# Optimization experiments

Hardware: AMD Instinct MI355X
Metric: run time of the kernel (lower is better)

Reference implementation:

```python
import jax, jax.numpy as jnp
import numpy as np

M_POS = 0.5
M_NEG_SIM = 0.1
LAM_NEG = 1.0


def setup_inputs() -> dict:
    key = jax.random.key(0)
    N, d, G = 8192, 1024, 64
    codebook = jax.random.normal(key, (N, d), dtype=jnp.float32)
    base = (jnp.arange(N) // G) * G  # contiguous groups of size G (vq_to_range)
    starts = base.astype(jnp.int32)
    ends = (base + G - 1).astype(jnp.int32)
    return {"codebook": codebook, "starts": starts, "ends": ends, "max_i": N - 1}


def reference(codebook, starts, ends, max_i):
    N, d = codebook.shape
    M = min(N, int(max_i) + 1)  # rows processed by the python loop

    # cosine similarity rows [0:M] vs all N
    zn = codebook / jnp.linalg.norm(codebook, axis=-1, keepdims=True)
    cos = jnp.einsum('md,nd->mn', zn[:M], zn)  # (M, N)

    # pairwise Euclidean distances rows [0:M] vs all N via ||a-b||^2 = |a|^2+|b|^2-2ab
    sq = jnp.sum(codebook * codebook, axis=-1)  # (N,)
    dot = jnp.einsum('md,nd->mn', codebook[:M], codebook)  # (M, N)
    d2 = jnp.maximum(sq[:M, None] + sq[None, :] - 2.0 * dot, 0.0)

    j = jnp.arange(N)[None, :]
    i = jnp.arange(M)[:, None]
    in_range = (j >= starts[:M, None]) & (j <= ends[:M, None])
    pos_mask = in_range & (j != i)
    # original: group_mask[i]=False then neg = ~group_mask, so i is in negatives
    neg_mask = (~in_range) | (j == i)

    pos_cnt = jnp.sum(pos_mask, axis=-1)
    neg_cnt = jnp.sum(neg_mask, axis=-1)

    # safe sqrt: only evaluate on positive-mask entries
    D = jnp.sqrt(jnp.where(pos_mask, d2, 1.0))
    pos_term = jnp.square(jax.nn.relu(D - M_POS)) * pos_mask
    pos_pull = jnp.sum(pos_term, axis=-1) / jnp.maximum(pos_cnt, 1)

    neg_cos = jnp.clip(cos, -1.0, 1.0)
    neg_term = jnp.square(jax.nn.relu(jnp.abs(neg_cos) - M_NEG_SIM)) * neg_mask
    ortho = jnp.sum(neg_term, axis=-1) / jnp.maximum(neg_cnt, 1)

    valid = (pos_cnt > 0) & (neg_cnt > 0)
    per_row = jnp.where(valid, pos_pull + LAM_NEG * ortho, 0.0)
    cnt = jnp.sum(valid)
    total = jnp.sum(per_row)
    return jnp.where(cnt > 0, total / jnp.maximum(cnt, 1).astype(total.dtype), jnp.zeros((), total.dtype))
```

## Files before the change

### kernel.cpp

```cpp
#include <hip/hip_runtime.h>
#include <hip/hip_bf16.h>
#include <stdint.h>

#define M_POS 0.5f
#define M_NEG 0.1f
#define LAM_NEG 1.0f

typedef __attribute__((ext_vector_type(4))) float floatx4;
typedef __attribute__((ext_vector_type(8))) int   intx8;

union Frag8 { intx8 v; int4 q[2]; };

__global__ __launch_bounds__(256) void prep_kernel(
    const float* __restrict__ cb, unsigned char* __restrict__ cb_q,
    float* __restrict__ sq, float* __restrict__ inv_norm,
    unsigned* __restrict__ zero_base, int zero_len,
    int N, int d)
{
    const int gi = blockIdx.x * 256 + threadIdx.x;
    if (gi < zero_len) zero_base[gi] = 0u;

    const int row = blockIdx.x;
    const float* src = cb + (size_t)row * d;
    unsigned char* dst = cb_q + (size_t)row * d;
    const int t = threadIdx.x;

    float s = 0.f;
    for (int c = t * 4; c < d; c += 1024) {
        float4 v = *(const float4*)(src + c);
        s += v.x * v.x + v.y * v.y + v.z * v.z + v.w * v.w;
        int pk = __builtin_amdgcn_cvt_pk_fp8_f32(v.x, v.y, 0, false);
        pk     = __builtin_amdgcn_cvt_pk_fp8_f32(v.z, v.w, pk, true);
        *(int*)(dst + c) = pk;
    }
    for (int o = 32; o > 0; o >>= 1) s += __shfl_down(s, o, 64);
    __shared__ float wsum[4];
    if ((t & 63) == 0) wsum[t >> 6] = s;
    __syncthreads();
    if (t == 0) {
        float tot = wsum[0] + wsum[1] + wsum[2] + wsum[3];
        sq[row] = tot;
        inv_norm[row] = rsqrtf(tot);
    }
}

__global__ __launch_bounds__(256, 2) void gram_loss_kernel(
    const unsigned char* __restrict__ A,
    const float* __restrict__ sq, const float* __restrict__ inv_norm,
    const int* __restrict__ starts, const int* __restrict__ ends,
    const int* __restrict__ max_ip,
    float* __restrict__ pos_acc, float* __restrict__ neg_acc,
    unsigned* __restrict__ counter, float* __restrict__ out,
    int N, int d)
{
    const int M = min(N, max_ip[0] + 1);

    int vt = blockIdx.x;
    const int nB = gridDim.x;
    if ((nB & 7) == 0) {
        const int per = nB >> 3;
        vt = (blockIdx.x & 7) * per + (blockIdx.x >> 3);
    }

    int bx = (int)((sqrtf(8.f * (float)vt + 1.f) - 1.f) * 0.5f);
    while ((bx + 1) * (bx + 2) / 2 <= vt) bx++;
    while (bx * (bx + 1) / 2 > vt) bx--;
    const int by = vt - bx * (bx + 1) / 2;

    const int rowBase = by * 128;
    const int colBase = bx * 128;
    const bool isDiag = (by == bx);

    __shared__ alignas(16) unsigned char ldsA[2][128 * 128];
    __shared__ alignas(16) unsigned char ldsB[2][128 * 128];

    const int tid  = threadIdx.x;
    const int wave = tid >> 6;
    const int lane = tid & 63;
    const int wr = (wave >> 1) * 64;
    const int wc = (wave & 1) * 64;

    floatx4 acc[4][4];
#pragma unroll
    for (int a = 0; a < 4; ++a)
#pragma unroll
        for (int b = 0; b < 4; ++b) acc[a][b] = (floatx4){0.f, 0.f, 0.f, 0.f};

    const int sRow = lane >> 3;
    const int sChk = lane & 7;
    const int srcOffC = ((sChk ^ sRow) * 16);
    const int kTiles = d / 128;

    const int rl = lane & 15;
    const int g  = lane >> 4;
    const int rx = rl & 7;
    const int c0 = (((2 * g)     ^ rx) * 16);
    const int c1 = (((2 * g + 1) ^ rx) * 16);

#define STAGE(BUF, KT)                                                          \
    { const int k0_ = (KT) * 128;                                               \
      _Pragma("unroll")                                                         \
      for (int h = 0; h < 4; ++h) {                                             \
        const int r_ = wave * 32 + h * 8 + sRow;                                \
        const unsigned char* ga_ = A + (size_t)(rowBase + r_) * d + k0_ + srcOffC; \
        const unsigned char* gb_ = A + (size_t)(colBase + r_) * d + k0_ + srcOffC; \
        __builtin_amdgcn_global_load_lds(                                       \
            (const __attribute__((address_space(1))) void*)ga_,                 \
            (__attribute__((address_space(3))) void*)(ldsA[BUF] + r_ * 128 + sChk * 16), 16, 0, 0); \
        __builtin_amdgcn_global_load_lds(                                       \
            (const __attribute__((address_space(1))) void*)gb_,                 \
            (__attribute__((address_space(3))) void*)(ldsB[BUF] + r_ * 128 + sChk * 16), 16, 0, 0); \
      } }

    STAGE(0, 0)
    asm volatile("s_waitcnt vmcnt(0)" ::: "memory");
    __builtin_amdgcn_s_barrier();

    int cur = 0;
    for (int kt = 0; kt < kTiles; ++kt) {
        const bool more = (kt + 1 < kTiles);
        if (more) {
            if (cur == 0) STAGE(1, kt + 1)
            else          STAGE(0, kt + 1)
        }

        Frag8 af[4], bf[4];
#pragma unroll
        for (int t4 = 0; t4 < 4; ++t4) {
            const unsigned char* pa = ldsA[cur] + (wr + t4 * 16 + rl) * 128;
            af[t4].q[0] = *(const int4*)(pa + c0);
            af[t4].q[1] = *(const int4*)(pa + c1);
            const unsigned char* pb = ldsB[cur] + (wc + t4 * 16 + rl) * 128;
            bf[t4].q[0] = *(const int4*)(pb + c0);
            bf[t4].q[1] = *(const int4*)(pb + c1);
        }
#pragma unroll
        for (int rt = 0; rt < 4; ++rt)
#pragma unroll
            for (int ct = 0; ct < 4; ++ct)
                acc[rt][ct] = __builtin_amdgcn_mfma_scale_f32_16x16x128_f8f6f4(
                    af[rt].v, bf[ct].v, acc[rt][ct], 0, 0, 0, 127, 0, 127);

        if (more) {
            asm volatile("s_waitcnt vmcnt(0)" ::: "memory");
            __builtin_amdgcn_s_barrier();
            cur ^= 1;
        }
    }
#undef STAGE

    const int q  = lane >> 4;
    const int jlo = colBase + wc;
    const int ilo = rowBase + wr;

    int   jn[4];
    float jinv[4];
    bool  jvalid[4];
#pragma unroll
    for (int ct = 0; ct < 4; ++ct) {
        const int j = jlo + ct * 16 + rl;
        jn[ct]  = j;
        jinv[ct] = inv_norm[j];
        jvalid[ct] = (j < M);
    }

    bool posLane = false;
    {
        const int ri = ilo + lane;
        if (ri < M) posLane |= (ends[ri] >= jlo) && (starts[ri] <= jlo + 63);
        if (!isDiag) {
            const int cj = jlo + lane;
            if (cj < M) posLane |= (ends[cj] >= ilo) && (starts[cj] <= ilo + 63);
        }
    }
    const bool fullPath = (__ballot(posLane) != 0ULL);

    float posc[4] = {0.f, 0.f, 0.f, 0.f};
    float negc[4] = {0.f, 0.f, 0.f, 0.f};

    if (fullPath) {
        int   jns[4], jne[4];
        float jsq[4];
#pragma unroll
        for (int ct = 0; ct < 4; ++ct) {
            jsq[ct] = sq[jn[ct]];
            jns[ct] = jvalid[ct] ? starts[jn[ct]] : 0;
            jne[ct] = jvalid[ct] ? ends[jn[ct]]   : -1;
        }
#pragma unroll
        for (int rt = 0; rt < 4; ++rt) {
            const int ibase = ilo + rt * 16 + q * 4;
#pragma unroll
            for (int reg = 0; reg < 4; ++reg) {
                const int i = ibase + reg;
                const bool rowValid = (i < M);
                const int ns = rowValid ? starts[i] : 0;
                const int ne = rowValid ? ends[i]   : -1;
                const float iinv = inv_norm[i];
                const float isq  = sq[i];
                float posp = 0.f, negp = 0.f;
#pragma unroll
                for (int ct = 0; ct < 4; ++ct) {
                    const float dot = acc[rt][ct][reg];
                    const int j = jn[ct];
                    float cosv = dot * iinv * jinv[ct];
                    cosv = fminf(fmaxf(cosv, -1.f), 1.f);
                    float tn = fmaxf(fabsf(cosv) - M_NEG, 0.f);
                    const float nterm = tn * tn;
                    const float d2 = fmaxf(isq + jsq[ct] - 2.f * dot, 0.f);
                    float tp = fmaxf(sqrtf(d2) - M_POS, 0.f);
                    const float pterm = tp * tp;
                    const bool dg = (j == i);
                    if (rowValid) {
                        const bool in_r = (j >= ns) && (j <= ne);
                        if (in_r && !dg) posp += pterm;
                        if (!in_r || dg) negp += nterm;
                    }
                    if (!isDiag && jvalid[ct]) {
                        const bool in_c = (i >= jns[ct]) && (i <= jne[ct]);
                        if (in_c && !dg) posc[ct] += pterm;
                        if (!in_c || dg) negc[ct] += nterm;
                    }
                }
#pragma unroll
                for (int m = 1; m < 16; m <<= 1) {
                    posp += __shfl_xor(posp, m, 64);
                    negp += __shfl_xor(negp, m, 64);
                }
                if (rowValid && rl == 0) {
                    atomicAdd(&pos_acc[i], posp);
                    atomicAdd(&neg_acc[i], negp);
                }
            }
        }
        if (!isDiag) {
#pragma unroll
            for (int ct = 0; ct < 4; ++ct) {
                posc[ct] += __shfl_xor(posc[ct], 16, 64);
                posc[ct] += __shfl_xor(posc[ct], 32, 64);
                negc[ct] += __shfl_xor(negc[ct], 16, 64);
                negc[ct] += __shfl_xor(negc[ct], 32, 64);
            }
            if (q == 0) {
#pragma unroll
                for (int ct = 0; ct < 4; ++ct) {
                    if (jvalid[ct]) {
                        atomicAdd(&pos_acc[jn[ct]], posc[ct]);
                        atomicAdd(&neg_acc[jn[ct]], negc[ct]);
                    }
                }
            }
        }
    } else {
#pragma unroll
        for (int rt = 0; rt < 4; ++rt) {
            const int ibase = ilo + rt * 16 + q * 4;
#pragma unroll
            for (int reg = 0; reg < 4; ++reg) {
                const int i = ibase + reg;
                const float iinv = inv_norm[i];
                float negp = 0.f;
#pragma unroll
                for (int ct = 0; ct < 4; ++ct) {
                    const float dot = acc[rt][ct][reg];
                    float cosv = dot * iinv * jinv[ct];
                    cosv = fminf(fmaxf(cosv, -1.f), 1.f);
                    float tn = fmaxf(fabsf(cosv) - M_NEG, 0.f);
                    const float nterm = tn * tn;
                    negp += nterm;
                    negc[ct] += nterm;
                }
#pragma unroll
                for (int m = 1; m < 16; m <<= 1)
                    negp += __shfl_xor(negp, m, 64);
                if ((i < M) && rl == 0)
                    atomicAdd(&neg_acc[i], negp);
            }
        }
        if (!isDiag) {
#pragma unroll
            for (int ct = 0; ct < 4; ++ct) {
                negc[ct] += __shfl_xor(negc[ct], 16, 64);
                negc[ct] += __shfl_xor(negc[ct], 32, 64);
            }
            if (q == 0) {
#pragma unroll
                for (int ct = 0; ct < 4; ++ct)
                    if (jvalid[ct])
                        atomicAdd(&neg_acc[jn[ct]], negc[ct]);
            }
        }
    }

    __shared__ bool amLast;
    __syncthreads();
    if (tid == 0) {
        __threadfence();
        unsigned old = atomicAdd(counter, 1u);
        amLast = (old == (unsigned)(gridDim.x - 1));
    }
    __syncthreads();
    if (amLast) {
        __threadfence();
        float total = 0.f;
        int cnt = 0;
        for (int i = tid; i < M; i += 256) {
            const float pa = __hip_atomic_load(&pos_acc[i], __ATOMIC_RELAXED, __HIP_MEMORY_SCOPE_AGENT);
            const float na = __hip_atomic_load(&neg_acc[i], __ATOMIC_RELAXED, __HIP_MEMORY_SCOPE_AGENT);
            const int ns = starts[i], ne = ends[i];
            const int lo = max(ns, 0), hi = min(ne, N - 1);
            const int inr = max(hi - lo + 1, 0);
            const bool dg = (i >= ns) && (i <= ne);
            const int pos_cnt = inr - (dg ? 1 : 0);
            const int neg_cnt = N - inr + (dg ? 1 : 0);
            if (pos_cnt > 0 && neg_cnt > 0) {
                total += pa / (float)max(pos_cnt, 1)
                       + LAM_NEG * na / (float)max(neg_cnt, 1);
                cnt++;
            }
        }
        for (int o = 32; o > 0; o >>= 1) {
            total += __shfl_down(total, o, 64);
            cnt   += __shfl_down(cnt, o, 64);
        }
        __shared__ float fin_ts[4];
        __shared__ int   fin_cs[4];
        if ((tid & 63) == 0) { fin_ts[tid >> 6] = total; fin_cs[tid >> 6] = cnt; }
        __syncthreads();
        if (tid == 0) {
            float T = fin_ts[0] + fin_ts[1] + fin_ts[2] + fin_ts[3];
            int   C = fin_cs[0] + fin_cs[1] + fin_cs[2] + fin_cs[3];
            out[0] = (C > 0) ? T / (float)C : 0.f;
        }
    }
}

extern "C" void kernel_launch(void* const* d_in, const int* in_sizes, int n_in,
                              void* d_out, int out_size, void* d_ws, size_t ws_size,
                              hipStream_t stream) {
    const float* cb     = (const float*)d_in[0];
    const int*   starts = (const int*)d_in[1];
    const int*   ends   = (const int*)d_in[2];
    const int*   max_ip = (const int*)d_in[3];
    float* out = (float*)d_out;

    const int N = in_sizes[1];
    const int d = in_sizes[0] / N;

    char* ws = (char*)d_ws;
    unsigned char* cb_q = (unsigned char*)ws;
    size_t off = ((size_t)N * d + 255) & ~(size_t)255;
    float* sq       = (float*)(ws + off); off += (size_t)N * 4;
    float* inv_norm = (float*)(ws + off); off += (size_t)N * 4;
    float* pos_acc  = (float*)(ws + off); off += (size_t)N * 4;
    float* neg_acc  = (float*)(ws + off); off += (size_t)N * 4;
    unsigned* counter = (unsigned*)(ws + off); off += 256;

    prep_kernel<<<N, 256, 0, stream>>>(cb, cb_q, sq, inv_norm,
                                       (unsigned*)pos_acc, 2 * N + 1, N, d);

    const int nb = N / 128;
    const int nBlocks = nb * (nb + 1) / 2;
    gram_loss_kernel<<<nBlocks, 256, 0, stream>>>(cb_q, sq, inv_norm, starts, ends,
                                                  max_ip, pos_acc, neg_acc, counter,
                                                  out, N, d);
}
```

Measured before the change: 232.2 us.

## Deepen gram K-loop to four-stage LDS pipeline and use one wave per prep row

The gram kernel's double-buffered K loop becomes a four-slot LDS ring. The first four K tiles are prefetched up front, and explicit vmcnt waits let later tiles load while earlier ones are computed. This needs 128 KB of LDS per block, so launch bounds drop to one block per CU and the finalisation scratch is carved out of the LDS buffers. The prep kernel now gives each wave one row, with 64-byte loads and 16-byte fp8 stores. That removes the block-level reduction and barrier, at the cost of more work per lane.

```diff
diff --git a/kernel.cpp b/kernel.cpp
--- a/kernel.cpp
+++ b/kernel.cpp
@@ -8,6 +8,7 @@
 
 typedef __attribute__((ext_vector_type(4))) float floatx4;
 typedef __attribute__((ext_vector_type(8))) int   intx8;
+typedef __attribute__((ext_vector_type(4))) int   int32x4;
 
 union Frag8 { intx8 v; int4 q[2]; };
 
@@ -20,31 +21,39 @@
     const int gi = blockIdx.x * 256 + threadIdx.x;
     if (gi < zero_len) zero_base[gi] = 0u;
 
-    const int row = blockIdx.x;
+    const int t = threadIdx.x;
+    const int w = t >> 6, l = t & 63;
+    const int row = blockIdx.x * 4 + w;
+    if (row >= N) return;
     const float* src = cb + (size_t)row * d;
     unsigned char* dst = cb_q + (size_t)row * d;
-    const int t = threadIdx.x;
 
     float s = 0.f;
-    for (int c = t * 4; c < d; c += 1024) {
-        float4 v = *(const float4*)(src + c);
-        s += v.x * v.x + v.y * v.y + v.z * v.z + v.w * v.w;
-        int pk = __builtin_amdgcn_cvt_pk_fp8_f32(v.x, v.y, 0, false);
-        pk     = __builtin_amdgcn_cvt_pk_fp8_f32(v.z, v.w, pk, true);
-        *(int*)(dst + c) = pk;
+    for (int c = l * 16; c < d; c += 1024) {
+        float4 v0 = *(const float4*)(src + c);
+        float4 v1 = *(const float4*)(src + c + 4);
+        float4 v2 = *(const float4*)(src + c + 8);
+        float4 v3 = *(const float4*)(src + c + 12);
+        s += v0.x*v0.x + v0.y*v0.y + v0.z*v0.z + v0.w*v0.w
+           + v1.x*v1.x + v1.y*v1.y + v1.z*v1.z + v1.w*v1.w
+           + v2.x*v2.x + v2.y*v2.y + v2.z*v2.z + v2.w*v2.w
+           + v3.x*v3.x + v3.y*v3.y + v3.z*v3.z + v3.w*v3.w;
+        int p0 = __builtin_amdgcn_cvt_pk_fp8_f32(v0.x, v0.y, 0, false);
+        p0     = __builtin_amdgcn_cvt_pk_fp8_f32(v0.z, v0.w, p0, true);
+        int p1 = __builtin_amdgcn_cvt_pk_fp8_f32(v1.x, v1.y, 0, false);
+        p1     = __builtin_amdgcn_cvt_pk_fp8_f32(v1.z, v1.w, p1, true);
+        int p2 = __builtin_amdgcn_cvt_pk_fp8_f32(v2.x, v2.y, 0, false);
+        p2     = __builtin_amdgcn_cvt_pk_fp8_f32(v2.z, v2.w, p2, true);
+        int p3 = __builtin_amdgcn_cvt_pk_fp8_f32(v3.x, v3.y, 0, false);
+        p3     = __builtin_amdgcn_cvt_pk_fp8_f32(v3.z, v3.w, p3, true);
+        int32x4 pk; pk.x = p0; pk.y = p1; pk.z = p2; pk.w = p3;
+        *(int32x4*)(dst + c) = pk;
     }
     for (int o = 32; o > 0; o >>= 1) s += __shfl_down(s, o, 64);
-    __shared__ float wsum[4];
-    if ((t & 63) == 0) wsum[t >> 6] = s;
-    __syncthreads();
-    if (t == 0) {
-        float tot = wsum[0] + wsum[1] + wsum[2] + wsum[3];
-        sq[row] = tot;
-        inv_norm[row] = rsqrtf(tot);
-    }
+    if (l == 0) { sq[row] = s; inv_norm[row] = rsqrtf(s); }
 }
 
-__global__ __launch_bounds__(256, 2) void gram_loss_kernel(
+__global__ __launch_bounds__(256, 1) void gram_loss_kernel(
     const unsigned char* __restrict__ A,
     const float* __restrict__ sq, const float* __restrict__ inv_norm,
     const int* __restrict__ starts, const int* __restrict__ ends,
@@ -71,8 +80,8 @@
     const int colBase = bx * 128;
     const bool isDiag = (by == bx);
 
-    __shared__ alignas(16) unsigned char ldsA[2][128 * 128];
-    __shared__ alignas(16) unsigned char ldsB[2][128 * 128];
+    __shared__ alignas(16) unsigned char ldsA[4][128 * 128];
+    __shared__ alignas(16) unsigned char ldsB[4][128 * 128];
 
     const int tid  = threadIdx.x;
     const int wave = tid >> 6;
@@ -97,7 +106,7 @@
     const int c0 = (((2 * g)     ^ rx) * 16);
     const int c1 = (((2 * g + 1) ^ rx) * 16);
 
-#define STAGE(BUF, KT)                                                          \
+#define STAGE(SLOT, KT)                                                         \
     { const int k0_ = (KT) * 128;                                               \
       _Pragma("unroll")                                                         \
       for (int h = 0; h < 4; ++h) {                                             \
@@ -106,48 +115,67 @@
         const unsigned char* gb_ = A + (size_t)(colBase + r_) * d + k0_ + srcOffC; \
         __builtin_amdgcn_global_load_lds(                                       \
             (const __attribute__((address_space(1))) void*)ga_,                 \
-            (__attribute__((address_space(3))) void*)(ldsA[BUF] + r_ * 128 + sChk * 16), 16, 0, 0); \
+            (__attribute__((address_space(3))) void*)(ldsA[SLOT] + r_ * 128 + sChk * 16), 16, 0, 0); \
         __builtin_amdgcn_global_load_lds(                                       \
             (const __attribute__((address_space(1))) void*)gb_,                 \
-            (__attribute__((address_space(3))) void*)(ldsB[BUF] + r_ * 128 + sChk * 16), 16, 0, 0); \
+            (__attribute__((address_space(3))) void*)(ldsB[SLOT] + r_ * 128 + sChk * 16), 16, 0, 0); \
       } }
 
-    STAGE(0, 0)
-    asm volatile("s_waitcnt vmcnt(0)" ::: "memory");
-    __builtin_amdgcn_s_barrier();
-
-    int cur = 0;
-    for (int kt = 0; kt < kTiles; ++kt) {
-        const bool more = (kt + 1 < kTiles);
-        if (more) {
-            if (cur == 0) STAGE(1, kt + 1)
-            else          STAGE(0, kt + 1)
-        }
-
-        Frag8 af[4], bf[4];
-#pragma unroll
-        for (int t4 = 0; t4 < 4; ++t4) {
-            const unsigned char* pa = ldsA[cur] + (wr + t4 * 16 + rl) * 128;
-            af[t4].q[0] = *(const int4*)(pa + c0);
-            af[t4].q[1] = *(const int4*)(pa + c1);
-            const unsigned char* pb = ldsB[cur] + (wc + t4 * 16 + rl) * 128;
-            bf[t4].q[0] = *(const int4*)(pb + c0);
-            bf[t4].q[1] = *(const int4*)(pb + c1);
-        }
-#pragma unroll
-        for (int rt = 0; rt < 4; ++rt)
-#pragma unroll
-            for (int ct = 0; ct < 4; ++ct)
-                acc[rt][ct] = __builtin_amdgcn_mfma_scale_f32_16x16x128_f8f6f4(
-                    af[rt].v, bf[ct].v, acc[rt][ct], 0, 0, 0, 127, 0, 127);
-
-        if (more) {
-            asm volatile("s_waitcnt vmcnt(0)" ::: "memory");
+#define COMPUTE(SLOT)                                                           \
+    { Frag8 af[4], bf[4];                                                       \
+      _Pragma("unroll")                                                         \
+      for (int t4 = 0; t4 < 4; ++t4) {                                          \
+        const unsigned char* pa = ldsA[SLOT] + (wr + t4 * 16 + rl) * 128;       \
+        af[t4].q[0] = *(const int4*)(pa + c0);                                  \
+        af[t4].q[1] = *(const int4*)(pa + c1);                                  \
+        const unsigned char* pb = ldsB[SLOT] + (wc + t4 * 16 + rl) * 128;       \
+        bf[t4].q[0] = *(const int4*)(pb + c0);                                  \
+        bf[t4].q[1] = *(const int4*)(pb + c1);                                  \
+      }                                                                         \
+      _Pragma("unroll")                                                         \
+      for (int rt = 0; rt < 4; ++rt)                                            \
+        _Pragma("unroll")                                                       \
+        for (int ct = 0; ct < 4; ++ct)                                          \
+          acc[rt][ct] = __builtin_amdgcn_mfma_scale_f32_16x16x128_f8f6f4(       \
+              af[rt].v, bf[ct].v, acc[rt][ct], 0, 0, 0, 127, 0, 127); }
+
+#define WAITV(NN)  asm volatile("s_waitcnt vmcnt(" #NN ")" ::: "memory")
+#define WAITL0     asm volatile("s_waitcnt lgkmcnt(0)" ::: "memory")
+
+    if (kTiles == 8) {
+        STAGE(0, 0) __builtin_amdgcn_sched_barrier(0);
+        STAGE(1, 1) __builtin_amdgcn_sched_barrier(0);
+        STAGE(2, 2) __builtin_amdgcn_sched_barrier(0);
+        STAGE(3, 3) __builtin_amdgcn_sched_barrier(0);
+#pragma unroll
+        for (int kt = 0; kt < 8; ++kt) {
+            if      (kt < 5)  WAITV(24);
+            else if (kt == 5) WAITV(16);
+            else if (kt == 6) WAITV(8);
+            else              WAITV(0);
             __builtin_amdgcn_s_barrier();
-            cur ^= 1;
+            COMPUTE(kt & 3)
+            if (kt + 4 < 8) {
+                WAITL0;
+                __builtin_amdgcn_s_barrier();
+                STAGE(kt & 3, kt + 4)
+                __builtin_amdgcn_sched_barrier(0);
+            }
+        }
+    } else {
+        for (int kt = 0; kt < kTiles; ++kt) {
+            STAGE(0, kt)
+            WAITV(0);
+            __builtin_amdgcn_s_barrier();
+            COMPUTE(0)
+            WAITL0;
+            __builtin_amdgcn_s_barrier();
         }
     }
 #undef STAGE
+#undef COMPUTE
+#undef WAITV
+#undef WAITL0
 
     const int q  = lane >> 4;
     const int jlo = colBase + wc;
@@ -292,15 +320,16 @@
         }
     }
 
-    __shared__ bool amLast;
+    struct FinSm { int amLast; float ts[4]; int cs[4]; };
+    FinSm* fs = (FinSm*)&ldsA[0][0];
     __syncthreads();
     if (tid == 0) {
         __threadfence();
         unsigned old = atomicAdd(counter, 1u);
-        amLast = (old == (unsigned)(gridDim.x - 1));
+        fs->amLast = (old == (unsigned)(gridDim.x - 1)) ? 1 : 0;
     }
     __syncthreads();
-    if (amLast) {
+    if (fs->amLast) {
         __threadfence();
         float total = 0.f;
         int cnt = 0;
@@ -323,13 +352,11 @@
             total += __shfl_down(total, o, 64);
             cnt   += __shfl_down(cnt, o, 64);
         }
-        __shared__ float fin_ts[4];
-        __shared__ int   fin_cs[4];
-        if ((tid & 63) == 0) { fin_ts[tid >> 6] = total; fin_cs[tid >> 6] = cnt; }
+        if ((tid & 63) == 0) { fs->ts[tid >> 6] = total; fs->cs[tid >> 6] = cnt; }
         __syncthreads();
         if (tid == 0) {
-            float T = fin_ts[0] + fin_ts[1] + fin_ts[2] + fin_ts[3];
-            int   C = fin_cs[0] + fin_cs[1] + fin_cs[2] + fin_cs[3];
+            float T = fs->ts[0] + fs->ts[1] + fs->ts[2] + fs->ts[3];
+            int   C = fs->cs[0] + fs->cs[1] + fs->cs[2] + fs->cs[3];
             out[0] = (C > 0) ? T / (float)C : 0.f;
         }
     }
@@ -356,8 +383,8 @@
     float* neg_acc  = (float*)(ws + off); off += (size_t)N * 4;
     unsigned* counter = (unsigned*)(ws + off); off += 256;
 
-    prep_kernel<<<N, 256, 0, stream>>>(cb, cb_q, sq, inv_norm,
-                                       (unsigned*)pos_acc, 2 * N + 1, N, d);
+    prep_kernel<<<(N + 3) / 4, 256, 0, stream>>>(cb, cb_q, sq, inv_norm,
+                                                 (unsigned*)pos_acc, 2 * N + 1, N, d);
 
     const int nb = N / 128;
     const int nBlocks = nb * (nb + 1) / 2;
```

Result: slower. 277.4 us (+19.5%).
